# Kernel tuning notes

Measured on AMD Instinct MI355X. Metric: run time of the kernel, lower is better.

## Reference

```python
import jax, jax.numpy as jnp
import numpy as np

NUM_EXPERTS = 8
AUX_LOSS_COEF = 0.01


def setup_inputs() -> dict:
    key = jax.random.key(0)
    ks = jax.random.split(key, 5)
    B, S, D, E, H = 4, 2048, 1024, NUM_EXPERTS, 4096
    scale = 0.02  # typical init scale so gelu/softmax stay in sane ranges
    return {
        "hidden_states": jax.random.normal(ks[0], (B, S, D), dtype=jnp.float32),
        "router_w": jax.random.normal(ks[1], (D, E), dtype=jnp.float32) * scale,
        "router_b": jnp.zeros((E,), dtype=jnp.float32),
        "w1": jax.random.normal(ks[2], (E, D, H), dtype=jnp.float32) * scale,
        "b1": jnp.zeros((E, H), dtype=jnp.float32),
        "w2": jax.random.normal(ks[3], (E, H, D), dtype=jnp.float32) * scale,
        "b2": jnp.zeros((E, D), dtype=jnp.float32),
    }


def reference(hidden_states, router_w, router_b, w1, b1, w2, b2):
    B, S, D = hidden_states.shape
    E = w1.shape[0]
    x = hidden_states.reshape(-1, D)  # [T, D] flattened tokens

    # Switch router: top-1 expert, combine weight = softmax prob of chosen expert
    logits = x @ router_w + router_b                      # [T, E]
    probs = jax.nn.softmax(logits, axis=-1)               # [T, E]
    sel = jnp.argmax(logits, axis=-1)                     # [T] int
    gate = jnp.take_along_axis(probs, sel[:, None], axis=1)[:, 0]  # [T]

    # Expert FFNs: per-expert Linear -> gelu -> Linear, masked top-1 combine.
    # Loop is over the small fixed expert count (structurally distinct weights).
    out = jnp.zeros_like(x)
    for e in range(E):
        h = jax.nn.gelu(x @ w1[e] + b1[e])                # [T, H]
        ye = h @ w2[e] + b2[e]                            # [T, D]
        mask = (sel == e).astype(x.dtype)
        out = out + (mask * gate)[:, None] * ye

    # Switch load-balancing auxiliary loss
    mean_probs = probs.mean(axis=0)                       # [E]
    assignments = jnp.mean(jax.nn.one_hot(sel, E, dtype=x.dtype), axis=0)  # [E]
    aux_loss = jnp.sum(mean_probs * assignments) * E
    total_loss = AUX_LOSS_COEF * aux_loss

    return out.reshape(B, S, D), total_loss
```

## Files before the change

### kernel.cpp

```cpp
#include <hip/hip_runtime.h>
#include <cstdint>

typedef __bf16 bf16_t;
typedef __attribute__((ext_vector_type(8))) __bf16 bf16x8;
typedef __attribute__((ext_vector_type(4))) float f32x4;
typedef unsigned short ushort_t;

#define TOKENS 8192
#define DIM 1024
#define HID 4096
#define NEXP 8

__device__ __forceinline__ void gl_lds16(const void* g, void* l) {
  __builtin_amdgcn_global_load_lds(
      (__attribute__((address_space(1))) void*)(void*)g,
      (__attribute__((address_space(3))) void*)l, 16, 0, 0);
}

__device__ __forceinline__ float gelu_tanh(float x) {
  float z = 0.7978845608028654f * (x + 0.044715f * x * x * x);
  z = fminf(fmaxf(z, -15.f), 15.f);
  float e = __expf(-2.f * z);
  float th = (1.f - e) / (1.f + e);
  return 0.5f * x * (1.f + th);
}

__global__ void router_kernel(const float* __restrict__ x, const float* __restrict__ rw,
                              const float* __restrict__ rbias, bf16_t* __restrict__ xb,
                              int* __restrict__ sel, float* __restrict__ gate,
                              float* __restrict__ pprob, int* __restrict__ pcnt) {
  __shared__ float sprob[NEXP];
  __shared__ int scnt[NEXP];
  int t = threadIdx.x, lane = t & 63, wave = t >> 6;
  if (t < NEXP) { sprob[t] = 0.f; scnt[t] = 0; }
  __syncthreads();
  int tok = blockIdx.x * 4 + wave;
  const float* xp = x + (size_t)tok * DIM + lane * 16;
  float acc[NEXP];
#pragma unroll
  for (int e = 0; e < NEXP; ++e) acc[e] = 0.f;
  ushort_t xv[16];
#pragma unroll
  for (int j = 0; j < 16; j += 4) {
    float4 v = *(const float4*)(xp + j);
    const float* wr = rw + (size_t)(lane * 16 + j) * NEXP;
    float c[4] = {v.x, v.y, v.z, v.w};
#pragma unroll
    for (int d = 0; d < 4; ++d) {
      xv[j + d] = __builtin_bit_cast(ushort_t, (bf16_t)c[d]);
#pragma unroll
      for (int e = 0; e < NEXP; ++e) acc[e] += c[d] * wr[d * NEXP + e];
    }
  }
  {
    uint4* xop = (uint4*)(xb + (size_t)tok * DIM + lane * 16);
    xop[0] = ((uint4*)xv)[0];
    xop[1] = ((uint4*)xv)[1];
  }
#pragma unroll
  for (int s = 1; s < 64; s <<= 1)
#pragma unroll
    for (int e = 0; e < NEXP; ++e) acc[e] += __shfl_xor(acc[e], s);
  if (lane == 0) {
    float lg[NEXP];
#pragma unroll
    for (int e = 0; e < NEXP; ++e) lg[e] = acc[e] + rbias[e];
    float mx = lg[0]; int am = 0;
#pragma unroll
    for (int e = 1; e < NEXP; ++e) if (lg[e] > mx) { mx = lg[e]; am = e; }
    float p[NEXP]; float se = 0.f;
#pragma unroll
    for (int e = 0; e < NEXP; ++e) { p[e] = __expf(lg[e] - mx); se += p[e]; }
    float inv = 1.f / se;
#pragma unroll
    for (int e = 0; e < NEXP; ++e) { p[e] *= inv; atomicAdd(&sprob[e], p[e]); }
    sel[tok] = am;
    gate[tok] = p[am];
    atomicAdd(&scnt[am], 1);
  }
  __syncthreads();
  if (t < NEXP) {
    pprob[blockIdx.x * NEXP + t] = sprob[t];
    pcnt[blockIdx.x * NEXP + t] = scnt[t];
  }
}

__global__ void tcvt2_kernel(const float* __restrict__ w1, const float* __restrict__ w2,
                             bf16_t* __restrict__ w1t, bf16_t* __restrict__ w2t) {
  __shared__ float tile[64][65];
  int y = blockIdx.y;
  int which = y >> 3, e = y & 7;
  int R = which ? HID : DIM;
  int C = which ? DIM : HID;
  const float* src = (which ? w2 : w1) + (size_t)e * R * C;
  bf16_t* dst = (which ? w2t : w1t) + (size_t)e * R * C;
  int cbt = C >> 6;
  int rt = blockIdx.x / cbt, ct = blockIdx.x % cbt;
  int rb = rt * 64, cb = ct * 64;
  int t = threadIdx.x;
  int r = t >> 2, cq = (t & 3) * 16;
  const float* sp = src + (size_t)(rb + r) * C + cb + cq;
#pragma unroll
  for (int j = 0; j < 16; j += 4) {
    float4 v = *(const float4*)(sp + j);
    tile[r][cq + j + 0] = v.x; tile[r][cq + j + 1] = v.y;
    tile[r][cq + j + 2] = v.z; tile[r][cq + j + 3] = v.w;
  }
  __syncthreads();
  int oc = t >> 2, orr = (t & 3) * 16;
  ushort_t tmp[16];
#pragma unroll
  for (int j = 0; j < 16; ++j) {
    bf16_t b = (bf16_t)tile[orr + j][oc];
    tmp[j] = __builtin_bit_cast(ushort_t, b);
  }
  uint4* dp = (uint4*)(dst + (size_t)(cb + oc) * R + rb + orr);
  dp[0] = ((uint4*)tmp)[0];
  dp[1] = ((uint4*)tmp)[1];
}

__global__ void reduce_kernel(const float* __restrict__ pprob, const int* __restrict__ pcnt,
                              int nb, int* __restrict__ counts, int* __restrict__ offsets,
                              int* __restrict__ cursors, float* __restrict__ loss_out) {
  __shared__ float fred[256];
  __shared__ int ired[256];
  int t = threadIdx.x;
  int e = t & 7, i0 = t >> 3;
  float fs = 0.f; int is = 0;
  for (int i = i0; i < nb; i += 32) { fs += pprob[i * 8 + e]; is += pcnt[i * 8 + e]; }
  fred[t] = fs; ired[t] = is;
  __syncthreads();
  if (t < NEXP) {
    float tp = 0.f; int tc = 0;
    for (int j = 0; j < 32; ++j) { tp += fred[j * 8 + t]; tc += ired[j * 8 + t]; }
    counts[t] = tc;
    fred[t] = tp;
    cursors[t] = 0;
  }
  __syncthreads();
  if (t == 0) {
    int off = 0; float loss = 0.f;
    for (int q = 0; q < NEXP; ++q) {
      offsets[q] = off; off += counts[q];
      loss += (fred[q] / (float)TOKENS) * ((float)counts[q] / (float)TOKENS);
    }
    *loss_out = loss * (float)NEXP * 0.01f;
  }
}

__global__ void scatter_kernel(const int* __restrict__ sel, const int* __restrict__ offsets,
                               int* __restrict__ cursors, int* __restrict__ idxl) {
  int tok = blockIdx.x * 256 + threadIdx.x;
  int lane = threadIdx.x & 63;
  int e = sel[tok];
#pragma unroll
  for (int ex = 0; ex < NEXP; ++ex) {
    unsigned long long mask = __ballot(e == ex);
    if (e == ex) {
      int leader = __ffsll(mask) - 1;
      int total = __popcll(mask);
      int rank = __popcll(mask & ((1ull << lane) - 1ull));
      int base = 0;
      if (lane == leader) base = atomicAdd(&cursors[ex], total);
      base = __shfl(base, leader);
      idxl[offsets[ex] + base + rank] = tok;
    }
  }
}

__global__ __launch_bounds__(256) void gemm1_kernel(
    const bf16_t* __restrict__ xb, const bf16_t* __restrict__ w1t,
    const float* __restrict__ b1, const int* __restrict__ idxl,
    const int* __restrict__ counts, const int* __restrict__ offsets,
    bf16_t* __restrict__ h) {
  int e = blockIdx.z;
  int cnt = counts[e];
  int mBase = blockIdx.y * 128;
  if (mBase >= cnt) return;
  int nBase = blockIdx.x * 128;
  int off = offsets[e];
  __shared__ bf16_t As[4096], Bs[4096];
  int t = threadIdx.x, lane = t & 63, wave = t >> 6;
  int wrow = wave >> 1, wcol = wave & 1;
  f32x4 acc[4][4];
#pragma unroll
  for (int m = 0; m < 4; ++m)
#pragma unroll
    for (int n = 0; n < 4; ++n) acc[m][n] = (f32x4){0.f, 0.f, 0.f, 0.f};

  int srow = wave * 16 + (lane >> 2);
  int kin = (lane & 3) * 8;
  int c1 = cnt - 1;
  int slot0 = mBase + srow; slot0 = slot0 < c1 ? slot0 : c1;
  int slot1 = mBase + srow + 64; slot1 = slot1 < c1 ? slot1 : c1;
  int tok0 = idxl[off + slot0], tok1 = idxl[off + slot1];
  const bf16_t* ag0 = xb + (size_t)tok0 * DIM + kin;
  const bf16_t* ag1 = xb + (size_t)tok1 * DIM + kin;
  const bf16_t* wb = w1t + (size_t)e * HID * DIM;
  const bf16_t* bg0 = wb + (size_t)(nBase + srow) * DIM + kin;
  const bf16_t* bg1 = bg0 + (size_t)64 * DIM;
  bf16_t* lA0 = As + wave * 512;
  bf16_t* lA1 = As + 2048 + wave * 512;
  bf16_t* lB0 = Bs + wave * 512;
  bf16_t* lB1 = Bs + 2048 + wave * 512;
  int kcol = (lane >> 4) * 8;

  for (int kt = 0; kt < DIM / 32; ++kt) {
    int k0 = kt * 32;
    gl_lds16(ag0 + k0, lA0);
    gl_lds16(ag1 + k0, lA1);
    gl_lds16(bg0 + k0, lB0);
    gl_lds16(bg1 + k0, lB1);
    __syncthreads();
    bf16x8 af[4], bv[4];
#pragma unroll
    for (int m = 0; m < 4; ++m)
      af[m] = *(const bf16x8*)(As + (wrow * 64 + m * 16 + (lane & 15)) * 32 + kcol);
#pragma unroll
    for (int n = 0; n < 4; ++n)
      bv[n] = *(const bf16x8*)(Bs + (wcol * 64 + n * 16 + (lane & 15)) * 32 + kcol);
#pragma unroll
    for (int m = 0; m < 4; ++m)
#pragma unroll
      for (int n = 0; n < 4; ++n)
        acc[m][n] = __builtin_amdgcn_mfma_f32_16x16x32_bf16(af[m], bv[n], acc[m][n], 0, 0, 0);
    __syncthreads();
  }

  float bias[4];
#pragma unroll
  for (int n = 0; n < 4; ++n) bias[n] = b1[e * HID + nBase + wcol * 64 + n * 16 + (lane & 15)];
#pragma unroll
  for (int m = 0; m < 4; ++m) {
    int rb0 = mBase + wrow * 64 + m * 16 + (lane >> 4) * 4;
#pragma unroll
    for (int j = 0; j < 4; ++j) {
      int r = rb0 + j;
      if (r < cnt) {
        bf16_t* hp = h + (size_t)(off + r) * HID + nBase + wcol * 64 + (lane & 15);
#pragma unroll
        for (int n = 0; n < 4; ++n)
          hp[n * 16] = (bf16_t)gelu_tanh(acc[m][n][j] + bias[n]);
      }
    }
  }
}

__global__ __launch_bounds__(256) void gemm2_kernel(
    const bf16_t* __restrict__ h, const bf16_t* __restrict__ w2t,
    const float* __restrict__ b2, const int* __restrict__ idxl,
    const float* __restrict__ gate, const int* __restrict__ counts,
    const int* __restrict__ offsets, float* __restrict__ out) {
  int e = blockIdx.z;
  int cnt = counts[e];
  int mBase = blockIdx.y * 64;
  if (mBase >= cnt) return;
  int nBase = blockIdx.x * 128;
  int off = offsets[e];
  __shared__ bf16_t S[6144];
  int t = threadIdx.x, lane = t & 63, wave = t >> 6;
  int wrow = wave >> 1, wcol = wave & 1;
  f32x4 acc[2][4];
#pragma unroll
  for (int m = 0; m < 2; ++m)
#pragma unroll
    for (int n = 0; n < 4; ++n) acc[m][n] = (f32x4){0.f, 0.f, 0.f, 0.f};

  int c1 = cnt - 1;
  int kin = (lane & 3) * 8;
  const bf16_t* srcp[3];
  bf16_t* ldst[3];
#pragma unroll
  for (int i = 0; i < 3; ++i) {
    int c = wave * 3 + i;
    int row = c * 16 + (lane >> 2);
    const bf16_t* p;
    if (row < 64) {
      int slot = mBase + row; slot = slot < c1 ? slot : c1;
      p = h + (size_t)(off + slot) * HID + kin;
    } else {
      p = w2t + (size_t)e * DIM * HID + (size_t)(nBase + row - 64) * HID + kin;
    }
    srcp[i] = p;
    ldst[i] = S + c * 512;
  }
  int kcol = (lane >> 4) * 8;

  for (int kt = 0; kt < HID / 32; ++kt) {
    int k0 = kt * 32;
    gl_lds16(srcp[0] + k0, ldst[0]);
    gl_lds16(srcp[1] + k0, ldst[1]);
    gl_lds16(srcp[2] + k0, ldst[2]);
    __syncthreads();
    bf16x8 af[2], bv[4];
#pragma unroll
    for (int m = 0; m < 2; ++m)
      af[m] = *(const bf16x8*)(S + (wrow * 32 + m * 16 + (lane & 15)) * 32 + kcol);
#pragma unroll
    for (int n = 0; n < 4; ++n)
      bv[n] = *(const bf16x8*)(S + 2048 + (wcol * 64 + n * 16 + (lane & 15)) * 32 + kcol);
#pragma unroll
    for (int m = 0; m < 2; ++m)
#pragma unroll
      for (int n = 0; n < 4; ++n)
        acc[m][n] = __builtin_amdgcn_mfma_f32_16x16x32_bf16(af[m], bv[n], acc[m][n], 0, 0, 0);
    __syncthreads();
  }

  float bias[4];
#pragma unroll
  for (int n = 0; n < 4; ++n) bias[n] = b2[e * DIM + nBase + wcol * 64 + n * 16 + (lane & 15)];
#pragma unroll
  for (int m = 0; m < 2; ++m) {
    int rb0 = mBase + wrow * 32 + m * 16 + (lane >> 4) * 4;
#pragma unroll
    for (int j = 0; j < 4; ++j) {
      int r = rb0 + j;
      if (r < cnt) {
        int tok = idxl[off + r];
        float g = gate[tok];
        float* op = out + (size_t)tok * DIM + nBase + wcol * 64 + (lane & 15);
#pragma unroll
        for (int n = 0; n < 4; ++n)
          op[n * 16] = g * (acc[m][n][j] + bias[n]);
      }
    }
  }
}

extern "C" void kernel_launch(void* const* d_in, const int* in_sizes, int n_in,
                              void* d_out, int out_size, void* d_ws, size_t ws_size,
                              hipStream_t stream) {
  const float* hs = (const float*)d_in[0];
  const float* rw = (const float*)d_in[1];
  const float* rb = (const float*)d_in[2];
  const float* w1 = (const float*)d_in[3];
  const float* b1 = (const float*)d_in[4];
  const float* w2 = (const float*)d_in[5];
  const float* b2 = (const float*)d_in[6];
  float* out = (float*)d_out;
  char* ws = (char*)d_ws;

  bf16_t* xb   = (bf16_t*)(ws + 0);
  bf16_t* w1t  = (bf16_t*)(ws + 16777216);
  bf16_t* w2t  = (bf16_t*)(ws + 83886080);
  bf16_t* hbuf = (bf16_t*)(ws + 150994944);
  int*   sel   = (int*)  (ws + 219152384);
  float* gate  = (float*)(ws + 219185152);
  int*   idxl  = (int*)  (ws + 219217920);
  float* pprob = (float*)(ws + 219250688);
  int*   pcnt  = (int*)  (ws + 219316224);
  int*   counts  = (int*)(ws + 219381760);
  int*   offsets = counts + 8;
  int*   cursors = counts + 16;

  router_kernel<<<2048, 256, 0, stream>>>(hs, rw, rb, xb, sel, gate, pprob, pcnt);
  tcvt2_kernel<<<dim3(1024, 16), 256, 0, stream>>>(w1, w2, w1t, w2t);
  reduce_kernel<<<1, 256, 0, stream>>>(pprob, pcnt, 2048, counts, offsets, cursors,
                                       out + (out_size - 1));
  scatter_kernel<<<32, 256, 0, stream>>>(sel, offsets, cursors, idxl);
  gemm1_kernel<<<dim3(32, 64, 8), 256, 0, stream>>>(xb, w1t, b1, idxl, counts, offsets, hbuf);
  gemm2_kernel<<<dim3(8, 128, 8), 256, 0, stream>>>(hbuf, w2t, b2, idxl, gate, counts, offsets, out);
}
```

Measured before the change: 434.9 us.

## Remap GEMM block order and enlarge gemm2 tile to 128x128 with 512 threads

Both expert GEMMs now remap the flat block index so that consecutive blocks cover different M tiles under the same N tile, with the aim of improving L2 reuse of weight columns. gemm2 moves from 64x128 tiles with 256 threads to 128x128 tiles with 512 threads (8 waves, each computing 64x32), halving the number of M blocks and the redundant reloads of w2. The trade-offs are fewer blocks, coarser padding waste on small expert counts, and higher per-block register and LDS use.

Measured after the change: 409.4 us. 5.9% less time.

```diff
diff --git a/kernel.cpp b/kernel.cpp
--- a/kernel.cpp
+++ b/kernel.cpp
@@ -175,9 +175,12 @@
     bf16_t* __restrict__ h) {
   int e = blockIdx.z;
   int cnt = counts[e];
-  int mBase = blockIdx.y * 128;
+  int f = blockIdx.y * 32 + blockIdx.x;
+  int lf = (f & 7) * 256 + (f >> 3);
+  int mt = lf & 63, nt = lf >> 6;
+  int mBase = mt * 128;
   if (mBase >= cnt) return;
-  int nBase = blockIdx.x * 128;
+  int nBase = nt * 128;
   int off = offsets[e];
   __shared__ bf16_t As[4096], Bs[4096];
   int t = threadIdx.x, lane = t & 63, wave = t >> 6;
@@ -246,82 +249,74 @@
   }
 }
 
-__global__ __launch_bounds__(256) void gemm2_kernel(
+__global__ __launch_bounds__(512) void gemm2_kernel(
     const bf16_t* __restrict__ h, const bf16_t* __restrict__ w2t,
     const float* __restrict__ b2, const int* __restrict__ idxl,
     const float* __restrict__ gate, const int* __restrict__ counts,
     const int* __restrict__ offsets, float* __restrict__ out) {
   int e = blockIdx.z;
   int cnt = counts[e];
-  int mBase = blockIdx.y * 64;
+  int f = blockIdx.y * 8 + blockIdx.x;
+  int lf = (f & 7) * 64 + (f >> 3);
+  int mt = lf & 63, nt = lf >> 6;
+  int mBase = mt * 128;
   if (mBase >= cnt) return;
-  int nBase = blockIdx.x * 128;
+  int nBase = nt * 128;
   int off = offsets[e];
-  __shared__ bf16_t S[6144];
+  __shared__ bf16_t S[8192];
   int t = threadIdx.x, lane = t & 63, wave = t >> 6;
-  int wrow = wave >> 1, wcol = wave & 1;
-  f32x4 acc[2][4];
-#pragma unroll
-  for (int m = 0; m < 2; ++m)
-#pragma unroll
-    for (int n = 0; n < 4; ++n) acc[m][n] = (f32x4){0.f, 0.f, 0.f, 0.f};
-
+  int wrow = wave >> 2, wcol = wave & 3;
+  f32x4 acc[4][2];
+#pragma unroll
+  for (int m = 0; m < 4; ++m)
+#pragma unroll
+    for (int n = 0; n < 2; ++n) acc[m][n] = (f32x4){0.f, 0.f, 0.f, 0.f};
+
+  int srow = wave * 16 + (lane >> 2);
+  int kin = (lane & 3) * 8;
   int c1 = cnt - 1;
-  int kin = (lane & 3) * 8;
-  const bf16_t* srcp[3];
-  bf16_t* ldst[3];
-#pragma unroll
-  for (int i = 0; i < 3; ++i) {
-    int c = wave * 3 + i;
-    int row = c * 16 + (lane >> 2);
-    const bf16_t* p;
-    if (row < 64) {
-      int slot = mBase + row; slot = slot < c1 ? slot : c1;
-      p = h + (size_t)(off + slot) * HID + kin;
-    } else {
-      p = w2t + (size_t)e * DIM * HID + (size_t)(nBase + row - 64) * HID + kin;
-    }
-    srcp[i] = p;
-    ldst[i] = S + c * 512;
-  }
+  int slot = mBase + srow; slot = slot < c1 ? slot : c1;
+  const bf16_t* agA = h + (size_t)(off + slot) * HID + kin;
+  const bf16_t* agB = w2t + (size_t)e * DIM * HID + (size_t)(nBase + srow) * HID + kin;
+  bf16_t* lA = S + wave * 512;
+  bf16_t* lB = S + 4096 + wave * 512;
   int kcol = (lane >> 4) * 8;
 
   for (int kt = 0; kt < HID / 32; ++kt) {
     int k0 = kt * 32;
-    gl_lds16(srcp[0] + k0, ldst[0]);
-    gl_lds16(srcp[1] + k0, ldst[1]);
-    gl_lds16(srcp[2] + k0, ldst[2]);
+    gl_lds16(agA + k0, lA);
+    gl_lds16(agB + k0, lB);
     __syncthreads();
-    bf16x8 af[2], bv[4];
-#pragma unroll
-    for (int m = 0; m < 2; ++m)
-      af[m] = *(const bf16x8*)(S + (wrow * 32 + m * 16 + (lane & 15)) * 32 + kcol);
-#pragma unroll
-    for (int n = 0; n < 4; ++n)
-      bv[n] = *(const bf16x8*)(S + 2048 + (wcol * 64 + n * 16 + (lane & 15)) * 32 + kcol);
-#pragma unroll
-    for (int m = 0; m < 2; ++m)
-#pragma unroll
-      for (int n = 0; n < 4; ++n)
+    bf16x8 af[4], bv[2];
+#pragma unroll
+    for (int m = 0; m < 4; ++m)
+      af[m] = *(const bf16x8*)(S + (wrow * 64 + m * 16 + (lane & 15)) * 32 + kcol);
+#pragma unroll
+    for (int n = 0; n < 2; ++n)
+      bv[n] = *(const bf16x8*)(S + 4096 + (wcol * 32 + n * 16 + (lane & 15)) * 32 + kcol);
+#pragma unroll
+    for (int m = 0; m < 4; ++m)
+#pragma unroll
+      for (int n = 0; n < 2; ++n)
         acc[m][n] = __builtin_amdgcn_mfma_f32_16x16x32_bf16(af[m], bv[n], acc[m][n], 0, 0, 0);
     __syncthreads();
   }
 
-  float bias[4];
-#pragma unroll
-  for (int n = 0; n < 4; ++n) bias[n] = b2[e * DIM + nBase + wcol * 64 + n * 16 + (lane & 15)];
-#pragma unroll
-  for (int m = 0; m < 2; ++m) {
-    int rb0 = mBase + wrow * 32 + m * 16 + (lane >> 4) * 4;
+  float bias[2];
+#pragma unroll
+  for (int n = 0; n < 2; ++n) bias[n] = b2[e * DIM + nBase + wcol * 32 + n * 16 + (lane & 15)];
+#pragma unroll
+  for (int m = 0; m < 4; ++m) {
+    int rb0 = mBase + wrow * 64 + m * 16 + (lane >> 4) * 4;
 #pragma unroll
     for (int j = 0; j < 4; ++j) {
       int r = rb0 + j;
       if (r < cnt) {
         int tok = idxl[off + r];
         float g = gate[tok];
-        float* op = out + (size_t)tok * DIM + nBase + wcol * 64 + (lane & 15);
-#pragma unroll
-        for (int n = 0; n < 4; ++n)
+        float* op = out + (size_t)tok * DIM + nBase + wcol * 32 + (lane & 15);
+#pragma unroll
+        for (int n = 0; n < 2; ++n)
           op[n * 16] = g * (acc[m][n][j] + bias[n]);
       }
     }
@@ -360,5 +355,5 @@
                                        out + (out_size - 1));
   scatter_kernel<<<32, 256, 0, stream>>>(sel, offsets, cursors, idxl);
   gemm1_kernel<<<dim3(32, 64, 8), 256, 0, stream>>>(xb, w1t, b1, idxl, counts, offsets, hbuf);
-  gemm2_kernel<<<dim3(8, 128, 8), 256, 0, stream>>>(hbuf, w2t, b2, idxl, gate, counts, offsets, out);
-}
+  gemm2_kernel<<<dim3(8, 64, 8), 512, 0, stream>>>(hbuf, w2t, b2, idxl, gate, counts, offsets, out);
+}
```
